# Kernel tuning notes

Measured on AMD Instinct MI355X. Metric: run time of the kernel, lower is better.

Reference implementation:

```python
import jax, jax.numpy as jnp
import numpy as np

D_IN = 768      # residual-stream width
D_SAE = 16384   # dictionary size
T = 4           # positions per window
K = 64          # TopK sparsity
PREFIX = (8192, 16384)  # prefix_sum for n_scales=2 even split
B = 1024


def setup_inputs() -> dict:
    key = jax.random.key(0)
    ks = jax.random.split(key, 6)
    x = jax.random.normal(ks[0], (B, T, D_IN), jnp.float32)
    # encoder weight ~ kaiming-uniform scale
    W_enc = jax.random.normal(ks[1], (T, D_IN, D_SAE), jnp.float32) * (1.0 / np.sqrt(D_IN))
    b_enc = jnp.zeros((D_SAE,), jnp.float32)
    # per-scale decoders, row-normalized over (T, d_in) as in _normalize_decoder
    def make_dec(k, prefix):
        W = jax.random.normal(k, (prefix, T, D_IN), jnp.float32)
        norms = jnp.linalg.norm(W.reshape(prefix, -1), axis=1).clip(1e-8)
        return W / norms[:, None, None]
    W_dec0 = make_dec(ks[2], PREFIX[0])
    W_dec1 = make_dec(ks[3], PREFIX[1])
    b_dec0 = jnp.zeros((T, D_IN), jnp.float32)
    b_dec1 = jnp.zeros((T, D_IN), jnp.float32)
    # non-identity per-position prefix permutation (T, d_sae)
    perm_keys = jax.random.split(ks[4], T)
    pos_prefix_perm = jax.vmap(lambda k: jax.random.permutation(k, D_SAE))(perm_keys).astype(jnp.int32)
    return {
        'x': x, 'W_enc': W_enc, 'b_enc': b_enc,
        'W_dec0': W_dec0, 'b_dec0': b_dec0,
        'W_dec1': W_dec1, 'b_dec1': b_dec1,
        'pos_prefix_perm': pos_prefix_perm,
    }


def reference(x, W_enc, b_enc, W_dec0, b_dec0, W_dec1, b_dec1, pos_prefix_perm):
    # ---- encode: pre-activation + per-row TopK + ReLU scatter into sparse code z
    pre = jnp.einsum('btd,tds->bs', x, W_enc) + b_enc            # (B, d_sae)
    vals, idx = jax.lax.top_k(pre, K)                            # (B, K)
    b = pre.shape[0]
    z = jnp.zeros_like(pre).at[jnp.arange(b)[:, None], idx].set(jax.nn.relu(vals))
    # ---- matryoshka per-(position, scale) reconstruction loss
    total = jnp.asarray(0.0, pre.dtype)
    x_hat_full = None
    for W, bd in ((W_dec0, b_dec0), (W_dec1, b_dec1)):
        prefix = W.shape[0]
        # position-dependent permutation gather: z_g[b,t,p] = z[b, perm[t,p]]
        z_g = z[:, pos_prefix_perm[:, :prefix]]                  # (B, T, prefix)
        x_hat = jnp.einsum('btp,ptd->btd', z_g, W) + bd          # (B, T, d_in)
        # sum over t of mean_b sum_d err^2  (== loop over t in the original)
        total = total + jnp.sum(jnp.mean(jnp.sum((x_hat - x) ** 2, axis=-1), axis=0))
        x_hat_full = x_hat
    total = total / (T * 2)  # divide by T * n_scales
    # aux-k loss: freshly initialized module has no dead latents
    # (num_tokens_since_fired starts at 0 << dead_threshold_tokens), so l_auxk == 0.
    return total, x_hat_full, z
```

## Files before the change

### kernel.cpp

```cpp
#include <hip/hip_runtime.h>
#include <hip/hip_bf16.h>
#include <stdint.h>

#define NB    1024
#define NT    4
#define NDIN  768
#define NSAE  16384
#define NK    64
#define KDIM  3072
#define PFX0  8192
#define KT96  96
#define VKD   6144
#define CCAP  2048

typedef _Float16 f16x8 __attribute__((ext_vector_type(8)));
typedef _Float16 f16x4 __attribute__((ext_vector_type(4)));
typedef float    f32x4 __attribute__((ext_vector_type(4)));

__device__ __forceinline__ unsigned f2key(float f) {
    union { float f; unsigned u; } cv; cv.f = f;
    unsigned u = cv.u;
    return u ^ ((unsigned)((int)u >> 31) | 0x80000000u);
}

__device__ __forceinline__ void ld16(const void* g, void* l) {
    __builtin_amdgcn_global_load_lds(
        (const __attribute__((address_space(1))) void*)g,
        (__attribute__((address_space(3))) void*)l, 16, 0, 0);
}

__global__ __launch_bounds__(256) void conv_a_kernel(
    const float* __restrict__ A, _Float16* __restrict__ A2)
{
    const int gid = blockIdx.x * 256 + threadIdx.x;
    const int m = gid / (KDIM / 4);
    const int k = (gid % (KDIM / 4)) * 4;
    const float4 v = *(const float4*)(A + (size_t)m * KDIM + k);
    const float vv[4] = { v.x, v.y, v.z, v.w };
    f16x4 h, l;
#pragma unroll
    for (int j = 0; j < 4; ++j) {
        const float sv = vv[j] * 64.f;
        const _Float16 hh = (_Float16)sv;
        h[j] = hh;
        l[j] = (_Float16)(sv - (float)hh);
    }
    const size_t ob = (size_t)m * VKD + (k >> 5) * 64 + (k & 31);
    *(f16x4*)(A2 + ob)      = h;
    *(f16x4*)(A2 + ob + 32) = l;
}

__global__ __launch_bounds__(512, 2) void gemm_f16split_kernel(
    const _Float16* __restrict__ A2, const float* __restrict__ Bsrc,
    const float* __restrict__ bias, float* __restrict__ pre)
{
    __shared__ _Float16 sA[2 * 256 * 64];
    __shared__ float    sB32[32 * 256];
    __shared__ _Float16 sBf[256 * 64];
    const int tid = threadIdx.x;
    const int lane = tid & 63;
    const int wid = tid >> 6;
    const int wm = wid >> 2;
    const int wn = wid & 3;

    const int bid = blockIdx.x;
    const int swz = (bid & 7) * 32 + (bid >> 3);
    const int m0 = (swz & 3) * 256;
    const int n0 = (swz >> 2) * 256;

    const _Float16* pa[4]; const float* pb[4];
    _Float16* da[4]; float* db[4];
#pragma unroll
    for (int r = 0; r < 4; ++r) {
        const int d = tid + r * 512;
        const int rowA = d >> 3;
        const int lsA = (d & 7) ^ (rowA & 7);
        pa[r] = A2 + (size_t)(m0 + rowA) * VKD + lsA * 8;
        da[r] = sA + d * 8;
        const int kB = d >> 6;
        const int slotB = d & 63;
        pb[r] = Bsrc + (size_t)kB * NSAE + n0 + slotB * 4;
        db[r] = sB32 + d * 4;
    }

    const int rl = lane & 15;
    const int qw = lane >> 4;
    const int off0 = ((0 + qw) ^ (rl & 7)) * 8 + rl * 64;
    const int off1 = ((4 + qw) ^ (rl & 7)) * 8 + rl * 64;

    const int cvn = tid & 255;
    const int cvkh = tid >> 8;
    const int cvsw = cvn & 7;
    _Float16* const cvout = sBf + cvn * 64;

    f32x4 acc[8][4];
#pragma unroll
    for (int mi = 0; mi < 8; ++mi)
#pragma unroll
        for (int ni = 0; ni < 4; ++ni)
            acc[mi][ni] = (f32x4){0.f, 0.f, 0.f, 0.f};

#pragma unroll
    for (int r = 0; r < 4; ++r) { ld16(pa[r], da[r]); ld16(pb[r], db[r]); }
    asm volatile("s_waitcnt vmcnt(0)" ::: "memory");
    __builtin_amdgcn_sched_barrier(0);
    __builtin_amdgcn_s_barrier();
    __builtin_amdgcn_sched_barrier(0);

    const size_t KSTRB = (size_t)32 * NSAE;

    for (int kt = 0; kt < KT96; ++kt) {
        const int cbA = (kt & 1) ? 16384 : 0;
        const int nbA = cbA ^ 16384;

        {
            float v[16];
#pragma unroll
            for (int j = 0; j < 16; ++j)
                v[j] = sB32[(cvkh * 16 + j) * 256 + cvn];
            f16x8 h0{}, h1{}, l0{}, l1{};
#pragma unroll
            for (int j = 0; j < 8; ++j) {
                const float sv = v[j] * 64.f;
                const _Float16 hh = (_Float16)sv;
                h0[j] = hh;
                l0[j] = (_Float16)(sv - (float)hh);
            }
#pragma unroll
            for (int j = 0; j < 8; ++j) {
                const float sv = v[8 + j] * 64.f;
                const _Float16 hh = (_Float16)sv;
                h1[j] = hh;
                l1[j] = (_Float16)(sv - (float)hh);
            }
            *(f16x8*)(cvout + (((cvkh * 2 + 0) ^ cvsw) * 8)) = h0;
            *(f16x8*)(cvout + (((cvkh * 2 + 1) ^ cvsw) * 8)) = h1;
            *(f16x8*)(cvout + (((4 + cvkh * 2 + 0) ^ cvsw) * 8)) = l0;
            *(f16x8*)(cvout + (((4 + cvkh * 2 + 1) ^ cvsw) * 8)) = l1;
        }
        asm volatile("s_waitcnt lgkmcnt(0)" ::: "memory");
        __builtin_amdgcn_sched_barrier(0);
        __builtin_amdgcn_s_barrier();
        __builtin_amdgcn_sched_barrier(0);

        if (kt + 1 < KT96) {
            const int koA = (kt + 1) * 64;
            const size_t koB = (size_t)(kt + 1) * KSTRB;
#pragma unroll
            for (int r = 0; r < 4; ++r) {
                ld16(pa[r] + koA, da[r] + nbA);
                ld16(pb[r] + koB, db[r]);
            }
        }
        __builtin_amdgcn_s_setprio(1);
        f16x8 bf[4][2];
#pragma unroll
        for (int ni = 0; ni < 4; ++ni) {
            const int rb = (wn * 64 + ni * 16) * 64;
            bf[ni][0] = *(const f16x8*)(sBf + rb + off0);
            bf[ni][1] = *(const f16x8*)(sBf + rb + off1);
        }
#pragma unroll
        for (int h = 0; h < 2; ++h) {
            f16x8 af[4][2];
#pragma unroll
            for (int i = 0; i < 4; ++i) {
                const int ra = cbA + (wm * 128 + (h * 4 + i) * 16) * 64;
                af[i][0] = *(const f16x8*)(sA + ra + off0);
                af[i][1] = *(const f16x8*)(sA + ra + off1);
            }
#pragma unroll
            for (int i = 0; i < 4; ++i)
#pragma unroll
                for (int ni = 0; ni < 4; ++ni) {
                    acc[h * 4 + i][ni] = __builtin_amdgcn_mfma_f32_16x16x32_f16(af[i][0], bf[ni][0], acc[h * 4 + i][ni], 0, 0, 0);
                    acc[h * 4 + i][ni] = __builtin_amdgcn_mfma_f32_16x16x32_f16(af[i][0], bf[ni][1], acc[h * 4 + i][ni], 0, 0, 0);
                    acc[h * 4 + i][ni] = __builtin_amdgcn_mfma_f32_16x16x32_f16(af[i][1], bf[ni][0], acc[h * 4 + i][ni], 0, 0, 0);
                }
        }
        __builtin_amdgcn_s_setprio(0);
        __builtin_amdgcn_sched_barrier(0);
        asm volatile("s_waitcnt vmcnt(0)" ::: "memory");
        __builtin_amdgcn_sched_barrier(0);
        __builtin_amdgcn_s_barrier();
        __builtin_amdgcn_sched_barrier(0);
    }

    const float c12 = 1.0f / 4096.0f;
    float bv[4];
#pragma unroll
    for (int ni = 0; ni < 4; ++ni) bv[ni] = bias[n0 + wn * 64 + ni * 16 + rl];
#pragma unroll
    for (int mi = 0; mi < 8; ++mi)
#pragma unroll
        for (int ni = 0; ni < 4; ++ni)
#pragma unroll
            for (int r = 0; r < 4; ++r) {
                const int row = m0 + wm * 128 + mi * 16 + qw * 4 + r;
                const int col = n0 + wn * 64 + ni * 16 + rl;
                pre[(size_t)row * NSAE + col] = acc[mi][ni][r] * c12 + bv[ni];
            }
}

__global__ __launch_bounds__(256) void gemm_pre_kernel(
    const float* __restrict__ A, const float* __restrict__ Bm,
    const float* __restrict__ bias, float* __restrict__ pre)
{
    __shared__ float As[16][128];
    __shared__ float Bs[16][128];
    const int bn = blockIdx.x * 128;
    const int bm = blockIdx.y * 128;
    const int tid = threadIdx.x;
    const int tx = tid & 15;
    const int ty = tid >> 4;

    float acc[8][8];
#pragma unroll
    for (int i = 0; i < 8; ++i)
#pragma unroll
        for (int j = 0; j < 8; ++j) acc[i][j] = 0.f;

    for (int k0 = 0; k0 < KDIM; k0 += 16) {
#pragma unroll
        for (int i = 0; i < 2; ++i) {
            const int idx = i * 256 + tid;
            const int r = idx >> 2;
            const int c = (idx & 3) << 2;
            const float4 v = *(const float4*)(A + (size_t)(bm + r) * KDIM + (k0 + c));
            As[c + 0][r] = v.x; As[c + 1][r] = v.y;
            As[c + 2][r] = v.z; As[c + 3][r] = v.w;
        }
#pragma unroll
        for (int i = 0; i < 2; ++i) {
            const int idx = i * 256 + tid;
            const int r = idx >> 5;
            const int c = (idx & 31) << 2;
            *(float4*)(&Bs[r][c]) = *(const float4*)(Bm + (size_t)(k0 + r) * NSAE + (bn + c));
        }
        __syncthreads();
#pragma unroll
        for (int kk = 0; kk < 16; ++kk) {
            const float4 a0 = *(const float4*)(&As[kk][ty * 8]);
            const float4 a1 = *(const float4*)(&As[kk][ty * 8 + 4]);
            const float4 b0 = *(const float4*)(&Bs[kk][tx * 8]);
            const float4 b1 = *(const float4*)(&Bs[kk][tx * 8 + 4]);
            const float av[8] = { a0.x, a0.y, a0.z, a0.w, a1.x, a1.y, a1.z, a1.w };
            const float bv[8] = { b0.x, b0.y, b0.z, b0.w, b1.x, b1.y, b1.z, b1.w };
#pragma unroll
            for (int i = 0; i < 8; ++i)
#pragma unroll
                for (int j = 0; j < 8; ++j)
                    acc[i][j] = fmaf(av[i], bv[j], acc[i][j]);
        }
        __syncthreads();
    }

    float bv8[8];
#pragma unroll
    for (int j = 0; j < 8; ++j) bv8[j] = bias[bn + tx * 8 + j];
#pragma unroll
    for (int i = 0; i < 8; ++i) {
        float4 o0, o1;
        o0.x = acc[i][0] + bv8[0]; o0.y = acc[i][1] + bv8[1];
        o0.z = acc[i][2] + bv8[2]; o0.w = acc[i][3] + bv8[3];
        o1.x = acc[i][4] + bv8[4]; o1.y = acc[i][5] + bv8[5];
        o1.z = acc[i][6] + bv8[6]; o1.w = acc[i][7] + bv8[7];
        const size_t off = (size_t)(bm + ty * 8 + i) * NSAE + bn + tx * 8;
        *(float4*)(pre + off) = o0;
        *(float4*)(pre + off + 4) = o1;
    }
}

__global__ __launch_bounds__(256) void topk_kernel(
    const float* __restrict__ pre,
    int* __restrict__ tk_idx, float* __restrict__ tk_val,
    float* __restrict__ z)
{
    __shared__ unsigned hist[4][256];
    __shared__ unsigned scan[257];
    __shared__ int   cand[CCAP];
    __shared__ float cval[CCAP];
    __shared__ int sel[NK];
    __shared__ float sval[NK];
    __shared__ int ties[256];
    __shared__ float tval[256];
    __shared__ unsigned sh_prefix, sh_want, sh_cnt, sh_tiecnt, sh_ccnt, sh_bsel;

    const int b = blockIdx.x;
    const int tid = threadIdx.x;
    const int w = tid >> 6;
    const float* row = pre + (size_t)b * NSAE;
    float* zrow = z + (size_t)b * NSAE;

    if (tid == 0) { sh_cnt = 0u; sh_tiecnt = 0u; sh_ccnt = 0u; }
    hist[0][tid] = 0u; hist[1][tid] = 0u; hist[2][tid] = 0u; hist[3][tid] = 0u;
    __syncthreads();

    float4 rv[16];
#pragma unroll
    for (int j = 0; j < 16; ++j) {
        const int i = tid * 4 + j * 1024;
        rv[j] = *(const float4*)(row + i);
        *(float4*)(zrow + i) = make_float4(0.f, 0.f, 0.f, 0.f);
        atomicAdd(&hist[w][f2key(rv[j].x) >> 24], 1u);
        atomicAdd(&hist[w][f2key(rv[j].y) >> 24], 1u);
        atomicAdd(&hist[w][f2key(rv[j].z) >> 24], 1u);
        atomicAdd(&hist[w][f2key(rv[j].w) >> 24], 1u);
    }
    __syncthreads();
    hist[0][tid] += hist[1][tid] + hist[2][tid] + hist[3][tid];
    __syncthreads();

    scan[tid] = hist[0][tid];
    if (tid == 0) scan[256] = 0u;
    __syncthreads();
    for (int s = 1; s < 256; s <<= 1) {
        const unsigned v = (tid + s < 256) ? scan[tid + s] : 0u;
        __syncthreads();
        scan[tid] += v;
        __syncthreads();
    }
    if (scan[tid] >= (unsigned)NK && scan[tid + 1] < (unsigned)NK) {
        sh_bsel = (unsigned)tid;
        sh_prefix = ((unsigned)tid << 24);
        sh_want = (unsigned)NK - scan[tid + 1];
    }
    __syncthreads();
    const unsigned bsel0 = sh_bsel;

#pragma unroll
    for (int j = 0; j < 16; ++j) {
        const float fv[4] = { rv[j].x, rv[j].y, rv[j].z, rv[j].w };
#pragma unroll
        for (int q = 0; q < 4; ++q) {
            const unsigned k = f2key(fv[q]);
            if ((k >> 24) >= bsel0) {
                const unsigned s = atomicAdd(&sh_ccnt, 1u);
                if (s < (unsigned)CCAP) {
                    cand[s] = tid * 4 + j * 1024 + q;
                    cval[s] = fv[q];
                }
            }
        }
    }
    __syncthreads();
    const int ccnt_raw = (int)sh_ccnt;
    const bool ovf = ccnt_raw > CCAP;
    const int ccnt = ovf ? 0 : ccnt_raw;

    for (int pass = 1; pass < 4; ++pass) {
        hist[0][tid] = 0u; hist[1][tid] = 0u; hist[2][tid] = 0u; hist[3][tid] = 0u;
        __syncthreads();
        const int shift = 24 - pass * 8;
        const unsigned mask = 0xFFFFFFFFu << (shift + 8);
        const unsigned pfx = sh_prefix;
        if (!ovf) {
            for (int i = tid; i < ccnt; i += 256) {
                const unsigned k = f2key(cval[i]);
                if ((k & mask) == pfx) atomicAdd(&hist[w][(k >> shift) & 0xFFu], 1u);
            }
        } else {
#pragma unroll
            for (int j = 0; j < 16; ++j) {
                const float fv[4] = { rv[j].x, rv[j].y, rv[j].z, rv[j].w };
#pragma unroll
                for (int q = 0; q < 4; ++q) {
                    const unsigned k = f2key(fv[q]);
                    if ((k & mask) == pfx) atomicAdd(&hist[w][(k >> shift) & 0xFFu], 1u);
                }
            }
        }
        __syncthreads();
        hist[0][tid] += hist[1][tid] + hist[2][tid] + hist[3][tid];
        __syncthreads();
        scan[tid] = hist[0][tid];
        if (tid == 0) scan[256] = 0u;
        __syncthreads();
        for (int s = 1; s < 256; s <<= 1) {
            const unsigned v = (tid + s < 256) ? scan[tid + s] : 0u;
            __syncthreads();
            scan[tid] += v;
            __syncthreads();
        }
        const unsigned want = sh_want;
        __syncthreads();
        if (scan[tid] >= want && scan[tid + 1] < want) {
            sh_prefix |= ((unsigned)tid << shift);
            sh_want = want - scan[tid + 1];
        }
        __syncthreads();
    }

    const unsigned T = sh_prefix;
    if (!ovf) {
        for (int i = tid; i < ccnt; i += 256) {
            const unsigned k = f2key(cval[i]);
            if (k > T) {
                const unsigned s = atomicAdd(&sh_cnt, 1u);
                sel[s] = cand[i];
                sval[s] = cval[i];
            } else if (k == T) {
                const unsigned s = atomicAdd(&sh_tiecnt, 1u);
                if (s < 256u) { ties[s] = cand[i]; tval[s] = cval[i]; }
            }
        }
    } else {
#pragma unroll
        for (int j = 0; j < 16; ++j) {
            const float fv[4] = { rv[j].x, rv[j].y, rv[j].z, rv[j].w };
#pragma unroll
            for (int q = 0; q < 4; ++q) {
                const unsigned k = f2key(fv[q]);
                if (k > T) {
                    const unsigned s = atomicAdd(&sh_cnt, 1u);
                    sel[s] = tid * 4 + j * 1024 + q;
                    sval[s] = fv[q];
                } else if (k == T) {
                    const unsigned s = atomicAdd(&sh_tiecnt, 1u);
                    if (s < 256u) { ties[s] = tid * 4 + j * 1024 + q; tval[s] = fv[q]; }
                }
            }
        }
    }
    __syncthreads();
    if (tid == 0) {
        const unsigned tc = sh_tiecnt;
        const int n = (int)(tc < 256u ? tc : 256u);
        for (int a = 1; a < n; ++a) {
            const int v = ties[a]; const float fv = tval[a]; int c = a;
            while (c > 0 && ties[c - 1] > v) {
                ties[c] = ties[c - 1]; tval[c] = tval[c - 1]; --c;
            }
            ties[c] = v; tval[c] = fv;
        }
        const int base = (int)sh_cnt;
        const int want = (int)sh_want;
        for (int j = 0; j < want && j < n; ++j) {
            sel[base + j] = ties[j]; sval[base + j] = tval[j];
        }
    }
    __syncthreads();
    if (tid < NK) {
        const int myi = sel[tid];
        int rank = 0;
#pragma unroll 1
        for (int j = 0; j < NK; ++j) rank += (sel[j] < myi) ? 1 : 0;
        const float v = fmaxf(sval[tid], 0.f);
        tk_idx[b * NK + rank] = myi;
        tk_val[b * NK + rank] = v;
        zrow[myi] = v;
    }
}

__global__ __launch_bounds__(256) void invperm_kernel(
    const int* __restrict__ perm, int* __restrict__ ipos)
{
    const int i = blockIdx.x * 256 + threadIdx.x;
    if (i < NT * NSAE) {
        const int t = i >> 14;
        ipos[t * NSAE + perm[i]] = i & (NSAE - 1);
    }
}

__global__ __launch_bounds__(256) void decode_kernel(
    const float* __restrict__ x,
    const int* __restrict__ tk_idx, const float* __restrict__ tk_val,
    const int* __restrict__ ipos,
    const float* __restrict__ Wd0, const float* __restrict__ bd0,
    const float* __restrict__ Wd1, const float* __restrict__ bd1,
    float* __restrict__ xhat, float* __restrict__ part0, float* __restrict__ part1)
{
    const int gbid = blockIdx.x;
    const int t = gbid >> 10;
    const int b = gbid & (NB - 1);
    const int bt = b * NT + t;
    const int tid = threadIdx.x;

    __shared__ int s_p[NK];
    __shared__ float s_v[NK];
    if (tid < NK) {
        const int s = tk_idx[b * NK + tid];
        s_v[tid] = tk_val[b * NK + tid];
        s_p[tid] = ipos[t * NSAE + s];
    }
    __syncthreads();

    float acc0[3], acc1[3];
#pragma unroll
    for (int r = 0; r < 3; ++r) {
        const int d = tid + 256 * r;
        acc0[r] = bd0[t * NDIN + d];
        acc1[r] = bd1[t * NDIN + d];
    }
    for (int j = 0; j < NK; ++j) {
        const int p = s_p[j];
        const float v = s_v[j];
        const float* w1 = Wd1 + ((size_t)p * NT + t) * NDIN;
#pragma unroll
        for (int r = 0; r < 3; ++r) acc1[r] = fmaf(v, w1[tid + 256 * r], acc1[r]);
        if (p < PFX0) {
            const float* w0 = Wd0 + ((size_t)p * NT + t) * NDIN;
#pragma unroll
            for (int r = 0; r < 3; ++r) acc0[r] = fmaf(v, w0[tid + 256 * r], acc0[r]);
        }
    }

    float e0 = 0.f, e1 = 0.f;
#pragma unroll
    for (int r = 0; r < 3; ++r) {
        const int d = tid + 256 * r;
        const float xv = x[(size_t)bt * NDIN + d];
        const float d0 = acc0[r] - xv;
        const float d1 = acc1[r] - xv;
        e0 = fmaf(d0, d0, e0);
        e1 = fmaf(d1, d1, e1);
        xhat[(size_t)bt * NDIN + d] = acc1[r];
    }

    __shared__ float r0[256];
    __shared__ float r1[256];
    r0[tid] = e0; r1[tid] = e1;
    __syncthreads();
    for (int w2 = 128; w2 > 0; w2 >>= 1) {
        if (tid < w2) { r0[tid] += r0[tid + w2]; r1[tid] += r1[tid + w2]; }
        __syncthreads();
    }
    if (tid == 0) { part0[bt] = r0[0]; part1[bt] = r1[0]; }
}

__global__ __launch_bounds__(256) void reduce_kernel(
    const float* __restrict__ part0, const float* __restrict__ part1,
    float* __restrict__ out_total)
{
    __shared__ double red[256];
    const int tid = threadIdx.x;
    double s = 0.0;
    for (int i = tid; i < NB * NT; i += 256)
        s += (double)part0[i] + (double)part1[i];
    red[tid] = s;
    __syncthreads();
    for (int w = 128; w > 0; w >>= 1) {
        if (tid < w) red[tid] += red[tid + w];
        __syncthreads();
    }
    if (tid == 0) out_total[0] = (float)(red[0] / ((double)NB * (double)(NT * 2)));
}

extern "C" void kernel_launch(void* const* d_in, const int* in_sizes, int n_in,
                              void* d_out, int out_size, void* d_ws, size_t ws_size,
                              hipStream_t stream)
{
    const float* x     = (const float*)d_in[0];
    const float* W_enc = (const float*)d_in[1];
    const float* b_enc = (const float*)d_in[2];
    const float* Wd0   = (const float*)d_in[3];
    const float* bd0   = (const float*)d_in[4];
    const float* Wd1   = (const float*)d_in[5];
    const float* bd1   = (const float*)d_in[6];
    const int*   perm  = (const int*)d_in[7];

    float* out       = (float*)d_out;
    float* out_total = out;
    float* out_xhat  = out + 1;
    float* out_z     = out + 1 + (size_t)NB * NT * NDIN;

    char* ws = (char*)d_ws;
    size_t off = 0;
    float* pre = (float*)(ws + off); off += (size_t)NB * NSAE * sizeof(float);

    const size_t szA2 = (size_t)NB * VKD * sizeof(_Float16);
    _Float16* A2 = (_Float16*)(ws + off);
    const size_t off_splits_end = off + szA2;

    const bool fast = (ws_size >= off_splits_end +
        ((size_t)NB * NK * 8 + (size_t)NT * NSAE * 4 + (size_t)NB * NT * 8));
    size_t tail = fast ? off_splits_end : off;
    int*   tk_idx = (int*)(ws + tail);   tail += (size_t)NB * NK * sizeof(int);
    float* tk_val = (float*)(ws + tail); tail += (size_t)NB * NK * sizeof(float);
    int*   ipos   = (int*)(ws + tail);   tail += (size_t)NT * NSAE * sizeof(int);
    float* part0  = (float*)(ws + tail); tail += (size_t)NB * NT * sizeof(float);
    float* part1  = (float*)(ws + tail);

    if (fast) {
        conv_a_kernel<<<(NB * KDIM) / (256 * 4), 256, 0, stream>>>(x, A2);
        gemm_f16split_kernel<<<256, 512, 0, stream>>>(A2, W_enc, b_enc, pre);
    } else {
        gemm_pre_kernel<<<dim3(NSAE / 128, NB / 128), 256, 0, stream>>>(x, W_enc, b_enc, pre);
    }
    invperm_kernel<<<(NT * NSAE) / 256, 256, 0, stream>>>(perm, ipos);
    topk_kernel<<<NB, 256, 0, stream>>>(pre, tk_idx, tk_val, out_z);
    decode_kernel<<<NB * NT, 256, 0, stream>>>(x, tk_idx, tk_val, ipos,
                                               Wd0, bd0, Wd1, bd1,
                                               out_xhat, part0, part1);
    reduce_kernel<<<1, 256, 0, stream>>>(part0, part1, out_total);
}
```

Before: 524.7 us.

## Warp-specialize GEMM with producer waves doing loads and B conversion

Adds two producer wavefronts to the encoder GEMM block. They issue all global loads and convert fp32 W_enc tiles into split-f16 hi/lo form in a double-buffered shared-memory area, while the eight compute waves only run MFMAs. The goal is to take load and conversion latency off the MFMA critical path and overlap them with compute. In exchange, two waves must convert a whole tile, shared memory use grows and the per-iteration barrier handshakes become more complex, which could leave the producers as the bottleneck.

Result: slower. 851.9 us (+62.4%).

```diff
diff --git a/kernel.cpp b/kernel.cpp
--- a/kernel.cpp
+++ b/kernel.cpp
@@ -50,49 +50,120 @@
     *(f16x4*)(A2 + ob + 32) = l;
 }
 
-__global__ __launch_bounds__(512, 2) void gemm_f16split_kernel(
+#define CONVERT_P(BFOFF)                                                      \
+    _Pragma("unroll")                                                         \
+    for (int s = 0; s < 4; ++s) {                                             \
+        const int u = ptid + 128 * s;                                         \
+        const int n = u & 255;                                                \
+        const int kh = u >> 8;                                                \
+        float v[16];                                                          \
+        _Pragma("unroll")                                                     \
+        for (int j = 0; j < 16; ++j)                                          \
+            v[j] = sB32[(kh * 16 + j) * 256 + n];                             \
+        f16x8 h0{}, h1{}, l0{}, l1{};                                         \
+        _Pragma("unroll")                                                     \
+        for (int j = 0; j < 8; ++j) {                                         \
+            const float sv = v[j] * 64.f;                                     \
+            const _Float16 hh = (_Float16)sv;                                 \
+            h0[j] = hh; l0[j] = (_Float16)(sv - (float)hh);                   \
+        }                                                                     \
+        _Pragma("unroll")                                                     \
+        for (int j = 0; j < 8; ++j) {                                         \
+            const float sv = v[8 + j] * 64.f;                                 \
+            const _Float16 hh = (_Float16)sv;                                 \
+            h1[j] = hh; l1[j] = (_Float16)(sv - (float)hh);                   \
+        }                                                                     \
+        _Float16* const cvout = sBf + (BFOFF) + n * 64;                       \
+        const int cvsw = n & 7;                                               \
+        *(f16x8*)(cvout + (((kh * 2 + 0) ^ cvsw) * 8)) = h0;                  \
+        *(f16x8*)(cvout + (((kh * 2 + 1) ^ cvsw) * 8)) = h1;                  \
+        *(f16x8*)(cvout + (((4 + kh * 2 + 0) ^ cvsw) * 8)) = l0;              \
+        *(f16x8*)(cvout + (((4 + kh * 2 + 1) ^ cvsw) * 8)) = l1;              \
+    }
+
+__global__ __launch_bounds__(640) void gemm_f16split_kernel(
     const _Float16* __restrict__ A2, const float* __restrict__ Bsrc,
     const float* __restrict__ bias, float* __restrict__ pre)
 {
     __shared__ _Float16 sA[2 * 256 * 64];
+    __shared__ _Float16 sBf[2 * 256 * 64];
     __shared__ float    sB32[32 * 256];
-    __shared__ _Float16 sBf[256 * 64];
     const int tid = threadIdx.x;
     const int lane = tid & 63;
     const int wid = tid >> 6;
-    const int wm = wid >> 2;
-    const int wn = wid & 3;
 
     const int bid = blockIdx.x;
     const int swz = (bid & 7) * 32 + (bid >> 3);
     const int m0 = (swz & 3) * 256;
     const int n0 = (swz >> 2) * 256;
 
-    const _Float16* pa[4]; const float* pb[4];
-    _Float16* da[4]; float* db[4];
-#pragma unroll
-    for (int r = 0; r < 4; ++r) {
-        const int d = tid + r * 512;
-        const int rowA = d >> 3;
-        const int lsA = (d & 7) ^ (rowA & 7);
-        pa[r] = A2 + (size_t)(m0 + rowA) * VKD + lsA * 8;
-        da[r] = sA + d * 8;
-        const int kB = d >> 6;
-        const int slotB = d & 63;
-        pb[r] = Bsrc + (size_t)kB * NSAE + n0 + slotB * 4;
-        db[r] = sB32 + d * 4;
-    }
-
+    const size_t KSTRB = (size_t)32 * NSAE;
+
+    if (wid >= 8) {
+        const int ptid = tid - 512;
+        const int lsA = (ptid & 7) ^ ((ptid >> 3) & 7);
+        const _Float16* paBase = A2 + (size_t)(m0 + (ptid >> 3)) * VKD + lsA * 8;
+        _Float16* const daBase = sA + ptid * 8;
+        const float* pbBase = Bsrc + (size_t)(ptid >> 6) * NSAE + n0 + (ptid & 63) * 4;
+        float* const dbBase = sB32 + ptid * 4;
+
+#pragma unroll
+        for (int r = 0; r < 16; ++r) {
+            ld16(paBase + (size_t)r * 16 * VKD, daBase + r * 1024);
+            ld16(pbBase + (size_t)r * 2 * NSAE, dbBase + r * 512);
+        }
+        asm volatile("s_waitcnt vmcnt(0)" ::: "memory");
+        __builtin_amdgcn_sched_barrier(0);
+        __builtin_amdgcn_s_barrier();
+        __builtin_amdgcn_sched_barrier(0);
+        CONVERT_P(0)
+        asm volatile("s_waitcnt lgkmcnt(0)" ::: "memory");
+        __builtin_amdgcn_sched_barrier(0);
+#pragma unroll
+        for (int r = 0; r < 16; ++r)
+            ld16(pbBase + KSTRB + (size_t)r * 2 * NSAE, dbBase + r * 512);
+        __builtin_amdgcn_sched_barrier(0);
+        __builtin_amdgcn_s_barrier();
+        __builtin_amdgcn_sched_barrier(0);
+
+        for (int kt = 0; kt < KT96; ++kt) {
+            if (kt + 1 < KT96) {
+                const int bfoff = ((kt + 1) & 1) * 16384;
+                const int saoff = ((kt + 1) & 1) * 16384;
+                asm volatile("s_waitcnt vmcnt(0)" ::: "memory");
+                __builtin_amdgcn_sched_barrier(0);
+                CONVERT_P(bfoff)
+                asm volatile("s_waitcnt lgkmcnt(0)" ::: "memory");
+                __builtin_amdgcn_sched_barrier(0);
+                const size_t koA = (size_t)(kt + 1) * 64;
+#pragma unroll
+                for (int r = 0; r < 16; ++r)
+                    ld16(paBase + koA + (size_t)r * 16 * VKD,
+                         daBase + saoff + r * 1024);
+                if (kt + 2 < KT96) {
+                    const size_t koB = (size_t)(kt + 2) * KSTRB;
+#pragma unroll
+                    for (int r = 0; r < 16; ++r)
+                        ld16(pbBase + koB + (size_t)r * 2 * NSAE, dbBase + r * 512);
+                    asm volatile("s_waitcnt vmcnt(16)" ::: "memory");
+                } else {
+                    asm volatile("s_waitcnt vmcnt(0)" ::: "memory");
+                }
+                __builtin_amdgcn_sched_barrier(0);
+            }
+            __builtin_amdgcn_s_barrier();
+            __builtin_amdgcn_sched_barrier(0);
+        }
+        return;
+    }
+
+    const int wm = wid >> 2;
+    const int wn = wid & 3;
     const int rl = lane & 15;
     const int qw = lane >> 4;
     const int off0 = ((0 + qw) ^ (rl & 7)) * 8 + rl * 64;
     const int off1 = ((4 + qw) ^ (rl & 7)) * 8 + rl * 64;
 
-    const int cvn = tid & 255;
-    const int cvkh = tid >> 8;
-    const int cvsw = cvn & 7;
-    _Float16* const cvout = sBf + cvn * 64;
-
     f32x4 acc[8][4];
 #pragma unroll
     for (int mi = 0; mi < 8; ++mi)
@@ -100,63 +171,17 @@
         for (int ni = 0; ni < 4; ++ni)
             acc[mi][ni] = (f32x4){0.f, 0.f, 0.f, 0.f};
 
-#pragma unroll
-    for (int r = 0; r < 4; ++r) { ld16(pa[r], da[r]); ld16(pb[r], db[r]); }
-    asm volatile("s_waitcnt vmcnt(0)" ::: "memory");
-    __builtin_amdgcn_sched_barrier(0);
+    __builtin_amdgcn_s_barrier();
     __builtin_amdgcn_s_barrier();
     __builtin_amdgcn_sched_barrier(0);
 
-    const size_t KSTRB = (size_t)32 * NSAE;
-
     for (int kt = 0; kt < KT96; ++kt) {
-        const int cbA = (kt & 1) ? 16384 : 0;
-        const int nbA = cbA ^ 16384;
-
-        {
-            float v[16];
-#pragma unroll
-            for (int j = 0; j < 16; ++j)
-                v[j] = sB32[(cvkh * 16 + j) * 256 + cvn];
-            f16x8 h0{}, h1{}, l0{}, l1{};
-#pragma unroll
-            for (int j = 0; j < 8; ++j) {
-                const float sv = v[j] * 64.f;
-                const _Float16 hh = (_Float16)sv;
-                h0[j] = hh;
-                l0[j] = (_Float16)(sv - (float)hh);
-            }
-#pragma unroll
-            for (int j = 0; j < 8; ++j) {
-                const float sv = v[8 + j] * 64.f;
-                const _Float16 hh = (_Float16)sv;
-                h1[j] = hh;
-                l1[j] = (_Float16)(sv - (float)hh);
-            }
-            *(f16x8*)(cvout + (((cvkh * 2 + 0) ^ cvsw) * 8)) = h0;
-            *(f16x8*)(cvout + (((cvkh * 2 + 1) ^ cvsw) * 8)) = h1;
-            *(f16x8*)(cvout + (((4 + cvkh * 2 + 0) ^ cvsw) * 8)) = l0;
-            *(f16x8*)(cvout + (((4 + cvkh * 2 + 1) ^ cvsw) * 8)) = l1;
-        }
-        asm volatile("s_waitcnt lgkmcnt(0)" ::: "memory");
-        __builtin_amdgcn_sched_barrier(0);
-        __builtin_amdgcn_s_barrier();
-        __builtin_amdgcn_sched_barrier(0);
-
-        if (kt + 1 < KT96) {
-            const int koA = (kt + 1) * 64;
-            const size_t koB = (size_t)(kt + 1) * KSTRB;
-#pragma unroll
-            for (int r = 0; r < 4; ++r) {
-                ld16(pa[r] + koA, da[r] + nbA);
-                ld16(pb[r] + koB, db[r]);
-            }
-        }
+        const int cb = (kt & 1) ? 16384 : 0;
         __builtin_amdgcn_s_setprio(1);
         f16x8 bf[4][2];
 #pragma unroll
         for (int ni = 0; ni < 4; ++ni) {
-            const int rb = (wn * 64 + ni * 16) * 64;
+            const int rb = cb + (wn * 64 + ni * 16) * 64;
             bf[ni][0] = *(const f16x8*)(sBf + rb + off0);
             bf[ni][1] = *(const f16x8*)(sBf + rb + off1);
         }
@@ -165,7 +190,7 @@
             f16x8 af[4][2];
 #pragma unroll
             for (int i = 0; i < 4; ++i) {
-                const int ra = cbA + (wm * 128 + (h * 4 + i) * 16) * 64;
+                const int ra = cb + (wm * 128 + (h * 4 + i) * 16) * 64;
                 af[i][0] = *(const f16x8*)(sA + ra + off0);
                 af[i][1] = *(const f16x8*)(sA + ra + off1);
             }
@@ -179,8 +204,6 @@
                 }
         }
         __builtin_amdgcn_s_setprio(0);
-        __builtin_amdgcn_sched_barrier(0);
-        asm volatile("s_waitcnt vmcnt(0)" ::: "memory");
         __builtin_amdgcn_sched_barrier(0);
         __builtin_amdgcn_s_barrier();
         __builtin_amdgcn_sched_barrier(0);
@@ -583,7 +606,7 @@
 
     if (fast) {
         conv_a_kernel<<<(NB * KDIM) / (256 * 4), 256, 0, stream>>>(x, A2);
-        gemm_f16split_kernel<<<256, 512, 0, stream>>>(A2, W_enc, b_enc, pre);
+        gemm_f16split_kernel<<<256, 640, 0, stream>>>(A2, W_enc, b_enc, pre);
     } else {
         gemm_pre_kernel<<<dim3(NSAE / 128, NB / 128), 256, 0, stream>>>(x, W_enc, b_enc, pre);
     }
```
